# Kernel optimization log

Measured on AMD Instinct MI355X. Metric: run time of the kernel, lower is better.

## Reference

```python
import jax, jax.numpy as jnp
from jax import lax
import numpy as np

# Dims
B_, CIN, COUT, T = 2, 64, 128, 8192
K, NM, N, DCONV, EXP = 5, 2, 16, 4, 2   # kernel, n_mamba, d_state, d_conv, expand
DI = EXP * COUT                          # d_inner = 256
DTR = (COUT + 15) // 16                  # dt_rank = 8
M = NM * 2                               # mamba instances (fwd+bwd per block)


def setup_inputs() -> dict:
    key = jax.random.key(0)
    ks = jax.random.split(key, 8)
    r = lambda k, s, sc=0.02: (jax.random.normal(k, s) * sc).astype(jnp.float32)
    return {
        "x": jax.random.normal(ks[0], (B_, CIN, T), dtype=jnp.float32),
        "conv_w": r(ks[1], (COUT, CIN, K), 0.05),
        "conv_b": jnp.zeros((COUT,), jnp.float32),
        "gn_g": jnp.ones((COUT,), jnp.float32),
        "gn_b": jnp.zeros((COUT,), jnp.float32),
        "prelu_a": jnp.full((1,), 0.25, jnp.float32),
        "ln_g": jnp.ones((NM, COUT), jnp.float32),
        "ln_b": jnp.zeros((NM, COUT), jnp.float32),
        "W_in": r(ks[2], (M, 2 * DI, COUT)),
        "conv1d_w": r(ks[3], (M, DI, 1, DCONV), 0.1),
        "conv1d_b": jnp.zeros((M, DI), jnp.float32),
        "W_xproj": r(ks[4], (M, DTR + 2 * N, DI)),
        "W_dt": r(ks[5], (M, DI, DTR), 0.1),
        "b_dt": jnp.full((M, DI), -4.0, jnp.float32),
        "A_log": jnp.broadcast_to(jnp.log(jnp.arange(1, N + 1, dtype=jnp.float32)), (M, DI, N)).copy(),
        "D_param": jnp.ones((M, DI), jnp.float32),
        "W_out": r(ks[6], (M, COUT, DI)),
    }


def _silu(x):
    return x * jax.nn.sigmoid(x)


def _layernorm(x, g, b, eps=1e-5):
    mu = x.mean(-1, keepdims=True)
    v = ((x - mu) ** 2).mean(-1, keepdims=True)
    return (x - mu) * lax.rsqrt(v + eps) * g + b


def _mamba(h, Wi, cw, cb, Wx, Wd, bd, Alog, Dp, Wo):
    # h: [B, L, d_model] -> [B, L, d_model]. Standard Mamba (S6) block.
    Bb, L, _ = h.shape
    xz = jnp.einsum('bld,ed->ble', h, Wi)               # [B,L,2*DI]
    xp, z = jnp.split(xz, 2, axis=-1)
    xc = jnp.transpose(xp, (0, 2, 1))                   # [B,DI,L]
    xc = lax.conv_general_dilated(xc, cw, (1,), [(DCONV - 1, 0)],
                                  feature_group_count=DI,
                                  dimension_numbers=('NCH', 'OIH', 'NCH')) + cb[None, :, None]
    u = _silu(jnp.transpose(xc, (0, 2, 1)))             # [B,L,DI]
    xdbl = jnp.einsum('bld,ed->ble', u, Wx)             # [B,L,DTR+2N]
    dt, Bm, Cm = jnp.split(xdbl, [DTR, DTR + N], axis=-1)
    delta = jax.nn.softplus(jnp.einsum('blr,dr->bld', dt, Wd) + bd)  # [B,L,DI]
    A = -jnp.exp(Alog)                                  # [DI,N]
    dA = jnp.exp(delta[..., None] * A)                  # [B,L,DI,N]
    dBu = (delta * u)[..., None] * Bm[:, :, None, :]    # [B,L,DI,N]

    def step(hc, inp):
        a, b, c = inp
        hc = a * hc + b                                  # [B,DI,N]
        return hc, jnp.einsum('bdn,bn->bd', hc, c)

    h0 = jnp.zeros((Bb, DI, N), dtype=h.dtype)
    _, ys = lax.scan(step, h0, (jnp.moveaxis(dA, 1, 0), jnp.moveaxis(dBu, 1, 0), jnp.moveaxis(Cm, 1, 0)))
    y = jnp.moveaxis(ys, 0, 1) + u * Dp                 # [B,L,DI]
    y = y * _silu(z)
    return jnp.einsum('ble,de->bld', y, Wo)


def reference(x, conv_w, conv_b, gn_g, gn_b, prelu_a, ln_g, ln_b, W_in,
              conv1d_w, conv1d_b, W_xproj, W_dt, b_dt, A_log, D_param, W_out):
    # Conv1d stride 2, padding K//2: [B,CIN,T] -> [B,COUT,T//2]
    h = lax.conv_general_dilated(x, conv_w, (2,), [(K // 2, K // 2)],
                                 dimension_numbers=('NCH', 'OIH', 'NCH')) + conv_b[None, :, None]
    # GroupNorm(1, COUT): normalize jointly over (C, T)
    mu = h.mean((1, 2), keepdims=True)
    v = ((h - mu) ** 2).mean((1, 2), keepdims=True)
    h = (h - mu) * lax.rsqrt(v + 1e-5) * gn_g[None, :, None] + gn_b[None, :, None]
    h = jnp.where(h >= 0, h, prelu_a[0] * h)            # PReLU (shared scalar)
    h = jnp.transpose(h, (0, 2, 1))                     # [B, L, C]
    for i in range(NM):
        hn = _layernorm(h, ln_g[i], ln_b[i])
        f, bw = 2 * i, 2 * i + 1
        yf = _mamba(hn, W_in[f], conv1d_w[f], conv1d_b[f], W_xproj[f], W_dt[f], b_dt[f], A_log[f], D_param[f], W_out[f])
        hb = jnp.flip(hn, axis=1)
        yb = jnp.flip(_mamba(hb, W_in[bw], conv1d_w[bw], conv1d_b[bw], W_xproj[bw], W_dt[bw], b_dt[bw], A_log[bw], D_param[bw], W_out[bw]), axis=1)
        h = h + yf + yb                                  # bidirectional residual
    return jnp.transpose(h, (0, 2, 1))                   # [B, COUT, T//2]
```

## Files before the change

kernel.cpp:

```cpp
#include <hip/hip_runtime.h>
#include <hip/hip_bf16.h>
#include <math.h>

constexpr int B2   = 2;
constexpr int CIN  = 64;
constexpr int COUT = 128;
constexpr int T    = 8192;
constexpr int L    = 4096;
constexpr int DI   = 256;
constexpr int NST  = 16;
constexpr int DTR  = 8;
constexpr int Q    = 32;
constexpr int NC   = 128;
constexpr int TOK  = B2 * L;

typedef __attribute__((ext_vector_type(8))) short bf16x8s;
typedef __attribute__((ext_vector_type(4))) float f32x4;

__device__ __forceinline__ float sigmoidf_(float x) { return 1.f / (1.f + __expf(-x)); }
__device__ __forceinline__ unsigned short f2bf(float f) {
    unsigned int u = __float_as_uint(f);
    unsigned int r = (u + 0x7FFFu + ((u >> 16) & 1u)) >> 16;
    return (unsigned short)r;
}
__device__ __forceinline__ float bf2f(unsigned short s) {
    return __uint_as_float((unsigned int)s << 16);
}

__global__ __launch_bounds__(256) void prep_all_kernel(
    const float* __restrict__ W_in, const float* __restrict__ W_out,
    const float* __restrict__ cw,
    unsigned short* __restrict__ Winb, unsigned short* __restrict__ Woutb,
    unsigned short* __restrict__ Wrb, float* __restrict__ stats) {
    int idx = blockIdx.x * 256 + threadIdx.x;
    if (blockIdx.x == 0 && threadIdx.x < 4) stats[threadIdx.x] = 0.f;
    if (idx < 262144) {
        Winb[idx] = f2bf(W_in[idx]);
    } else if (idx < 393216) {
        int i = idx - 262144; Woutb[i] = f2bf(W_out[i]);
    } else if (idx < 434176) {
        int i = idx - 393216;
        int co = i / 320, r = i % 320;
        int kp = r >> 6, ci = r & 63;
        Wrb[i] = f2bf(cw[co * 320 + ci * 5 + kp]);
    }
}

__global__ __launch_bounds__(256) void xpose_kernel(
    const float* __restrict__ x, unsigned short* __restrict__ xTb) {
    __shared__ float tile[64][65];
    int b = blockIdx.y, tb = blockIdx.x * 64, tid = threadIdx.x;
    #pragma unroll
    for (int i = 0; i < 16; ++i) {
        int idx = i * 256 + tid; int ci = idx >> 6, tt = idx & 63;
        tile[ci][tt] = x[((size_t)b * CIN + ci) * T + tb + tt];
    }
    __syncthreads();
    #pragma unroll
    for (int i = 0; i < 16; ++i) {
        int idx = i * 256 + tid; int tt = idx >> 6, ci = idx & 63;
        xTb[((size_t)b * T + tb + tt) * 64 + ci] = f2bf(tile[ci][tt]);
    }
}

__global__ __launch_bounds__(256) void conv_mfma_kernel(
    const unsigned short* __restrict__ xTb, const unsigned short* __restrict__ Wrb,
    const float* __restrict__ cb, float* __restrict__ h, float* __restrict__ stats) {
    const int tid = threadIdx.x;
    const int w = tid >> 6, lane = tid & 63, q = lane >> 4, c = lane & 15;
    const int t0g = blockIdx.x * 64;
    const int t0  = t0g + w * 16;
    const int ct0 = blockIdx.y * 64;
    const int b   = t0g >> 12;
    const int l   = (t0 + c) & (L - 1);
    f32x4 acc[4] = {};
    for (int kc = 0; kc < 320; kc += 32) {
        int kp  = kc >> 6;
        int ci0 = (kc & 63) + q * 8;
        int p = 2 * l + kp - 2;
        bf16x8s a = {};
        if (p >= 0 && p < T)
            a = *(const bf16x8s*)&xTb[((size_t)b * T + p) * 64 + ci0];
        #pragma unroll
        for (int i = 0; i < 4; ++i) {
            bf16x8s bb = *(const bf16x8s*)&Wrb[(size_t)(ct0 + i * 16 + c) * 320 + kc + q * 8];
            acc[i] = __builtin_amdgcn_mfma_f32_16x16x32_bf16(a, bb, acc[i], 0, 0, 0);
        }
    }
    float s = 0.f, ss = 0.f;
    #pragma unroll
    for (int i = 0; i < 4; ++i) {
        int cout = ct0 + i * 16 + c;
        float bias = cb[cout];
        #pragma unroll
        for (int r = 0; r < 4; ++r) {
            int tok = t0 + q * 4 + r;
            float v = acc[i][r] + bias;
            h[(size_t)tok * COUT + cout] = v;
            s += v; ss += v * v;
        }
    }
    #pragma unroll
    for (int off = 32; off; off >>= 1) {
        s  += __shfl_down(s,  off, 64);
        ss += __shfl_down(ss, off, 64);
    }
    if (lane == 0) {
        atomicAdd(&stats[b * 2 + 0], s);
        atomicAdd(&stats[b * 2 + 1], ss);
    }
}

__global__ __launch_bounds__(256) void gn_ln_kernel(
    float* __restrict__ h, const float* __restrict__ gn_g,
    const float* __restrict__ gn_b, const float* __restrict__ prelu_a,
    const float* __restrict__ stats, unsigned short* __restrict__ hnb,
    const float* __restrict__ lng, const float* __restrict__ lnb) {
    int wave = threadIdx.x >> 6, lane = threadIdx.x & 63;
    int t = blockIdx.x * 4 + wave;
    int b = t >> 12;
    const float n = (float)(L * COUT);
    float mu   = stats[b * 2 + 0] / n;
    float var  = stats[b * 2 + 1] / n - mu * mu;
    float rstd = rsqrtf(var + 1e-5f);
    float a = prelu_a[0];
    float* row = h + (size_t)t * COUT;
    float2 v  = *(const float2*)&row[lane * 2];
    float2 g  = *(const float2*)&gn_g[lane * 2];
    float2 bb = *(const float2*)&gn_b[lane * 2];
    v.x = (v.x - mu) * rstd * g.x + bb.x; v.x = v.x >= 0.f ? v.x : a * v.x;
    v.y = (v.y - mu) * rstd * g.y + bb.y; v.y = v.y >= 0.f ? v.y : a * v.y;
    *(float2*)&row[lane * 2] = v;
    float s = v.x + v.y, ss = v.x * v.x + v.y * v.y;
    #pragma unroll
    for (int off = 32; off; off >>= 1) {
        s  += __shfl_xor(s,  off, 64);
        ss += __shfl_xor(ss, off, 64);
    }
    float mu2 = s * (1.f / 128.f);
    float var2 = ss * (1.f / 128.f) - mu2 * mu2;
    float rstd2 = rsqrtf(var2 + 1e-5f);
    float2 gg = *(const float2*)&lng[lane * 2];
    float2 lb = *(const float2*)&lnb[lane * 2];
    ushort2 o;
    o.x = f2bf((v.x - mu2) * rstd2 * gg.x + lb.x);
    o.y = f2bf((v.y - mu2) * rstd2 * gg.y + lb.y);
    *(ushort2*)&hnb[(size_t)t * COUT + lane * 2] = o;
}

__global__ __launch_bounds__(256) void ln_kernel(
    const float* __restrict__ h, unsigned short* __restrict__ hnb,
    const float* __restrict__ g, const float* __restrict__ bta) {
    int wave = threadIdx.x >> 6, lane = threadIdx.x & 63;
    int t = blockIdx.x * 4 + wave;
    const float* row = h + (size_t)t * COUT;
    float2 v = *(const float2*)&row[lane * 2];
    float s = v.x + v.y, ss = v.x * v.x + v.y * v.y;
    #pragma unroll
    for (int off = 32; off; off >>= 1) {
        s  += __shfl_xor(s,  off, 64);
        ss += __shfl_xor(ss, off, 64);
    }
    float mu = s * (1.f / 128.f);
    float var = ss * (1.f / 128.f) - mu * mu;
    float rstd = rsqrtf(var + 1e-5f);
    float2 gg = *(const float2*)&g[lane * 2];
    float2 bb = *(const float2*)&bta[lane * 2];
    ushort2 o;
    o.x = f2bf((v.x - mu) * rstd * gg.x + bb.x);
    o.y = f2bf((v.y - mu) * rstd * gg.y + bb.y);
    *(ushort2*)&hnb[(size_t)t * COUT + lane * 2] = o;
}

__global__ __launch_bounds__(256) void inproj_dw_kernel(
    const unsigned short* __restrict__ hnb, const unsigned short* __restrict__ Winb,
    const float* __restrict__ cw, const float* __restrict__ cbias,
    float* __restrict__ u0, float* __restrict__ u1,
    unsigned short* __restrict__ zb0, unsigned short* __restrict__ zb1, int layer) {
    __shared__ float xs[80 * 68];
    const int tid = threadIdx.x;
    const int w = tid >> 6, lane = tid & 63, q = lane >> 4, c = lane & 15;
    const int tBase = blockIdx.x * 64;
    const int nBase = blockIdx.y * 64;
    const int inst = nBase >> 9;
    const int e0 = nBase & 511;
    const int m = layer * 2 + inst;
    const unsigned short* Wb = Winb + (size_t)m * 512 * 128;

    if (e0 >= 256) {
        const int t0 = tBase + w * 16;
        f32x4 acc[4] = {};
        for (int kc = 0; kc < 128; kc += 32) {
            bf16x8s a = *(const bf16x8s*)&hnb[(size_t)(t0 + c) * 128 + kc + q * 8];
            #pragma unroll
            for (int i = 0; i < 4; ++i) {
                bf16x8s bb = *(const bf16x8s*)&Wb[(size_t)(e0 + i * 16 + c) * 128 + kc + q * 8];
                acc[i] = __builtin_amdgcn_mfma_f32_16x16x32_bf16(a, bb, acc[i], 0, 0, 0);
            }
        }
        unsigned short* zb = inst ? zb1 : zb0;
        #pragma unroll
        for (int i = 0; i < 4; ++i) {
            int eo = (e0 + i * 16 + c) & 255;
            #pragma unroll
            for (int r = 0; r < 4; ++r) {
                int tok = t0 + q * 4 + r;
                float v = acc[i][r];
                zb[(size_t)tok * DI + eo] = f2bf(v * sigmoidf_(v));
            }
        }
        return;
    }
    const int winT0 = (inst == 0) ? (tBase - 16) : tBase;
    for (int pass = 0; pass < 2; ++pass) {
        if (pass == 1 && w != 0) break;
        int slot = (pass == 0) ? (w + (inst == 0 ? 1 : 0))
                               : ((inst == 0) ? 0 : 4);
        int tokA = winT0 + slot * 16 + c;
        tokA = tokA < 0 ? 0 : (tokA > TOK - 1 ? TOK - 1 : tokA);
        f32x4 acc[4] = {};
        for (int kc = 0; kc < 128; kc += 32) {
            bf16x8s a = *(const bf16x8s*)&hnb[(size_t)tokA * 128 + kc + q * 8];
            #pragma unroll
            for (int i = 0; i < 4; ++i) {
                bf16x8s bb = *(const bf16x8s*)&Wb[(size_t)(e0 + i * 16 + c) * 128 + kc + q * 8];
                acc[i] = __builtin_amdgcn_mfma_f32_16x16x32_bf16(a, bb, acc[i], 0, 0, 0);
            }
        }
        #pragma unroll
        for (int i = 0; i < 4; ++i)
            #pragma unroll
            for (int r = 0; r < 4; ++r)
                xs[(slot * 16 + q * 4 + r) * 68 + i * 16 + c] = acc[i][r];
    }
    __syncthreads();
    const int l0base = tBase & (L - 1);
    const int ch4 = tid & 15;
    const int d0 = e0 + ch4 * 4;
    float4 w0 = *(const float4*)&cw[(size_t)(m * DI + d0 + 0) * 4];
    float4 w1 = *(const float4*)&cw[(size_t)(m * DI + d0 + 1) * 4];
    float4 w2 = *(const float4*)&cw[(size_t)(m * DI + d0 + 2) * 4];
    float4 w3 = *(const float4*)&cw[(size_t)(m * DI + d0 + 3) * 4];
    float4 bias4 = *(const float4*)&cbias[m * DI + d0];
    float* ud = inst ? u1 : u0;
    #pragma unroll
    for (int p = 0; p < 4; ++p) {
        int j = p * 16 + (tid >> 4);
        float4 acc = bias4;
        #pragma unroll
        for (int k = 0; k < 4; ++k) {
            bool valid = (inst == 0) ? (l0base + j - 3 + k >= 0)
                                     : (l0base + j + 3 - k < L);
            if (valid) {
                int wj = (inst == 0) ? (j + 13 + k) : (j + 3 - k);
                float4 v = *(const float4*)&xs[wj * 68 + ch4 * 4];
                float wk0 = ((const float*)&w0)[k], wk1 = ((const float*)&w1)[k];
                float wk2 = ((const float*)&w2)[k], wk3 = ((const float*)&w3)[k];
                acc.x = fmaf(wk0, v.x, acc.x); acc.y = fmaf(wk1, v.y, acc.y);
                acc.z = fmaf(wk2, v.z, acc.z); acc.w = fmaf(wk3, v.w, acc.w);
            }
        }
        acc.x *= sigmoidf_(acc.x); acc.y *= sigmoidf_(acc.y);
        acc.z *= sigmoidf_(acc.z); acc.w *= sigmoidf_(acc.w);
        *(float4*)&ud[(size_t)(tBase + j) * DI + d0] = acc;
    }
}

__global__ __launch_bounds__(256) void xproj_kernel(
    const float* __restrict__ u0, const float* __restrict__ u1,
    const float* __restrict__ Wx, const float* __restrict__ Wdt,
    const float* __restrict__ bdt,
    float* __restrict__ dl0, float* __restrict__ dl1,
    float* __restrict__ Bm0, float* __restrict__ Bm1,
    float* __restrict__ Cm0, float* __restrict__ Cm1, int layer) {
    __shared__ float Ws[40 * 132];
    __shared__ float As[128 * 33];
    __shared__ float xd[32 * 9];
    const int tid   = threadIdx.x;
    const int tBase = blockIdx.x * 32;
    const int inst  = blockIdx.y;
    const int m     = layer * 2 + inst;
    const float* u  = inst ? u1 : u0;
    const float* Wm = Wx + (size_t)m * 40 * 256;
    const int t  = tid & 31;
    const int eq = tid >> 5;
    float acc[5] = {};
    for (int kc = 0; kc < 256; kc += 128) {
        __syncthreads();
        #pragma unroll
        for (int i = 0; i < 5; ++i) {
            int idx = i * 256 + tid;
            int e = idx >> 5, kq = idx & 31;
            float4 w4 = *(const float4*)&Wm[(size_t)e * 256 + kc + kq * 4];
            float* dstw = &Ws[e * 132 + kq * 4];
            dstw[0] = w4.x; dstw[1] = w4.y; dstw[2] = w4.z; dstw[3] = w4.w;
        }
        #pragma unroll
        for (int i = 0; i < 4; ++i) {
            int flat = i * 256 + tid;
            int tt = flat >> 5, kq = flat & 31;
            float4 v = *(const float4*)&u[(size_t)(tBase + tt) * DI + kc + kq * 4];
            As[(kq * 4 + 0) * 33 + tt] = v.x;
            As[(kq * 4 + 1) * 33 + tt] = v.y;
            As[(kq * 4 + 2) * 33 + tt] = v.z;
            As[(kq * 4 + 3) * 33 + tt] = v.w;
        }
        __syncthreads();
        #pragma unroll 4
        for (int kk = 0; kk < 128; ++kk) {
            float a = As[kk * 33 + t];
            acc[0] = fmaf(a, Ws[(eq     ) * 132 + kk], acc[0]);
            acc[1] = fmaf(a, Ws[(eq +  8) * 132 + kk], acc[1]);
            acc[2] = fmaf(a, Ws[(eq + 16) * 132 + kk], acc[2]);
            acc[3] = fmaf(a, Ws[(eq + 24) * 132 + kk], acc[3]);
            acc[4] = fmaf(a, Ws[(eq + 32) * 132 + kk], acc[4]);
        }
    }
    {
        int tok = tBase + t;
        float* Bm = inst ? Bm1 : Bm0;
        float* Cm = inst ? Cm1 : Cm0;
        xd[t * 9 + eq] = acc[0];
        Bm[(size_t)tok * NST + eq]     = acc[1];
        Bm[(size_t)tok * NST + 8 + eq] = acc[2];
        Cm[(size_t)tok * NST + eq]     = acc[3];
        Cm[(size_t)tok * NST + 8 + eq] = acc[4];
    }
    __syncthreads();
    {
        int d = tid;
        float wr[8];
        #pragma unroll
        for (int r = 0; r < 8; ++r) wr[r] = Wdt[((size_t)m * DI + d) * DTR + r];
        float bb = bdt[m * DI + d];
        float* dl = inst ? dl1 : dl0;
        #pragma unroll 4
        for (int tt = 0; tt < 32; ++tt) {
            float a2 = bb;
            #pragma unroll
            for (int r = 0; r < 8; ++r) a2 = fmaf(xd[tt * 9 + r], wr[r], a2);
            float sp = fmaxf(a2, 0.f) + __logf(1.f + __expf(-fabsf(a2)));
            dl[(size_t)(tBase + tt) * DI + d] = sp;
        }
    }
}

__global__ __launch_bounds__(256) void scan1_kernel(
    const float* __restrict__ dl0, const float* __restrict__ dl1,
    const float* __restrict__ u0,  const float* __restrict__ u1,
    const float* __restrict__ Bm0, const float* __restrict__ Bm1,
    const float* __restrict__ A_log,
    float* __restrict__ hend, float* __restrict__ dsumb, int layer) {
    const int tid = threadIdx.x;
    const int nq = tid & 3, dlane = tid >> 2;
    const int chunk = blockIdx.x & (NC - 1), dtile = blockIdx.x >> 7;
    const int b = blockIdx.y, inst = blockIdx.z;
    const int m = layer * 2 + inst, dir = inst;
    const int d = dtile * 64 + dlane;
    const float* dl = inst ? dl1 : dl0;
    const float* u  = inst ? u1  : u0;
    const float* Bm = inst ? Bm1 : Bm0;
    float4 av = *(const float4*)&A_log[((size_t)m * DI + d) * NST + nq * 4];
    const float a0 = -expf(av.x), a1 = -expf(av.y), a2 = -expf(av.z), a3 = -expf(av.w);
    const int s0 = chunk * Q;
    const int l0 = dir ? (L - 1 - s0) : s0;
    const int stp = dir ? -1 : 1;
    long iDU = ((long)(b * L + l0)) * DI + d;
    int  iB  = ((b * L + l0) << 4) + nq * 4;
    const long sDU = (long)stp * DI;
    const int  sB  = stp * NST;
    float h0 = 0.f, h1 = 0.f, h2 = 0.f, h3 = 0.f, dsum = 0.f;
    #pragma unroll 4
    for (int t = 0; t < Q; ++t) {
        float dlt = dl[iDU], uu = u[iDU];
        float4 bm = *(const float4*)&Bm[iB];
        float du = dlt * uu;
        h0 = fmaf(__expf(dlt * a0), h0, du * bm.x);
        h1 = fmaf(__expf(dlt * a1), h1, du * bm.y);
        h2 = fmaf(__expf(dlt * a2), h2, du * bm.z);
        h3 = fmaf(__expf(dlt * a3), h3, du * bm.w);
        dsum += dlt;
        iDU += sDU; iB += sB;
    }
    size_t oh = (((size_t)(inst * 2 + b) * DI + d) * NC + chunk) * NST + nq * 4;
    *(float4*)&hend[oh] = make_float4(h0, h1, h2, h3);
    if (nq == 0) dsumb[((size_t)(inst * 2 + b) * NC + chunk) * DI + d] = dsum;
}

__global__ __launch_bounds__(256) void combine_kernel(
    float* __restrict__ hend, const float* __restrict__ dsumb,
    const float* __restrict__ A_log, int layer) {
    int flat = blockIdx.x * 256 + threadIdx.x;
    int n = flat & 15;
    int d = (flat >> 4) & 255;
    int b = (flat >> 12) & 1;
    int inst = flat >> 13;
    int m = layer * 2 + inst;
    float a = -expf(A_log[((size_t)m * DI + d) * NST + n]);
    size_t baseE = (((size_t)(inst * 2 + b) * DI + d) * NC) * NST + n;
    size_t baseD = ((size_t)(inst * 2 + b) * NC) * DI + d;
    float hc = 0.f;
    #pragma unroll 4
    for (int c = 0; c < NC; ++c) {
        float tmp = hend[baseE + (size_t)c * NST];
        hend[baseE + (size_t)c * NST] = hc;
        float ds = dsumb[baseD + (size_t)c * DI];
        hc = fmaf(__expf(a * ds), hc, tmp);
    }
}

__global__ __launch_bounds__(256) void scan2_kernel(
    const float* __restrict__ dl0, const float* __restrict__ dl1,
    const float* __restrict__ u0,  const float* __restrict__ u1,
    const float* __restrict__ Bm0, const float* __restrict__ Bm1,
    const float* __restrict__ Cm0, const float* __restrict__ Cm1,
    unsigned short* __restrict__ zb0, unsigned short* __restrict__ zb1,
    const float* __restrict__ hin, const float* __restrict__ A_log,
    const float* __restrict__ Dp, int layer) {
    const int tid = threadIdx.x;
    const int nq = tid & 3, dlane = tid >> 2;
    const int chunk = blockIdx.x & (NC - 1), dtile = blockIdx.x >> 7;
    const int b = blockIdx.y, inst = blockIdx.z;
    const int m = layer * 2 + inst, dir = inst;
    const int d = dtile * 64 + dlane;
    const float* dl = inst ? dl1 : dl0;
    const float* u  = inst ? u1  : u0;
    const float* Bm = inst ? Bm1 : Bm0;
    const float* Cm = inst ? Cm1 : Cm0;
    unsigned short* zs = inst ? zb1 : zb0;
    float4 av = *(const float4*)&A_log[((size_t)m * DI + d) * NST + nq * 4];
    const float a0 = -expf(av.x), a1 = -expf(av.y), a2 = -expf(av.z), a3 = -expf(av.w);
    const float dpar = Dp[m * DI + d];
    const int s0 = chunk * Q;
    const int l0 = dir ? (L - 1 - s0) : s0;
    const int stp = dir ? -1 : 1;
    long iDU = ((long)(b * L + l0)) * DI + d;
    int  iB  = ((b * L + l0) << 4) + nq * 4;
    const long sDU = (long)stp * DI;
    const int  sB  = stp * NST;
    float4 hv = *(const float4*)&hin[(((size_t)(inst * 2 + b) * DI + d) * NC + chunk) * NST + nq * 4];
    float h0 = hv.x, h1 = hv.y, h2 = hv.z, h3 = hv.w;
    #pragma unroll 4
    for (int t = 0; t < Q; ++t) {
        float dlt = dl[iDU], uu = u[iDU];
        float4 bm = *(const float4*)&Bm[iB];
        float4 cm = *(const float4*)&Cm[iB];
        float du = dlt * uu;
        h0 = fmaf(__expf(dlt * a0), h0, du * bm.x);
        h1 = fmaf(__expf(dlt * a1), h1, du * bm.y);
        h2 = fmaf(__expf(dlt * a2), h2, du * bm.z);
        h3 = fmaf(__expf(dlt * a3), h3, du * bm.w);
        float yp = h0 * cm.x + h1 * cm.y + h2 * cm.z + h3 * cm.w;
        yp += __shfl_xor(yp, 1, 4);
        yp += __shfl_xor(yp, 2, 4);
        if (nq == 0) {
            float zv = bf2f(zs[iDU]);
            zs[iDU] = f2bf(fmaf(uu, dpar, yp) * zv);
        }
        iDU += sDU; iB += sB;
    }
}

__global__ __launch_bounds__(256) void outproj_mfma_kernel(
    const unsigned short* __restrict__ ygb0, const unsigned short* __restrict__ ygb1,
    const unsigned short* __restrict__ Woutb, float* __restrict__ h,
    float* __restrict__ out, int layer) {
    const int tid = threadIdx.x;
    const int w = tid >> 6, lane = tid & 63, q = lane >> 4, c = lane & 15;
    const int t0 = blockIdx.x * 64 + w * 16;
    const int ct0 = blockIdx.y * 32;
    f32x4 acc[2] = {};
    #pragma unroll
    for (int inst = 0; inst < 2; ++inst) {
        const unsigned short* yg = inst ? ygb1 : ygb0;
        const unsigned short* Wb = Woutb + (size_t)(layer * 2 + inst) * COUT * DI;
        for (int kc = 0; kc < 256; kc += 32) {
            bf16x8s a = *(const bf16x8s*)&yg[(size_t)(t0 + c) * DI + kc + q * 8];
            #pragma unroll
            for (int i = 0; i < 2; ++i) {
                bf16x8s bb = *(const bf16x8s*)&Wb[(size_t)(ct0 + i * 16 + c) * DI + kc + q * 8];
                acc[i] = __builtin_amdgcn_mfma_f32_16x16x32_bf16(a, bb, acc[i], 0, 0, 0);
            }
        }
    }
    if (layer == 0) {
        #pragma unroll
        for (int i = 0; i < 2; ++i) {
            int cout = ct0 + i * 16 + c;
            #pragma unroll
            for (int r = 0; r < 4; ++r) {
                int tok = t0 + q * 4 + r;
                h[(size_t)tok * COUT + cout] += acc[i][r];
            }
        }
    } else {
        int tok0 = t0 + q * 4;
        int b = tok0 >> 12, l = tok0 & (L - 1);
        #pragma unroll
        for (int i = 0; i < 2; ++i) {
            int cout = ct0 + i * 16 + c;
            float4 o;
            o.x = h[(size_t)(tok0 + 0) * COUT + cout] + acc[i][0];
            o.y = h[(size_t)(tok0 + 1) * COUT + cout] + acc[i][1];
            o.z = h[(size_t)(tok0 + 2) * COUT + cout] + acc[i][2];
            o.w = h[(size_t)(tok0 + 3) * COUT + cout] + acc[i][3];
            *(float4*)&out[((size_t)(b * COUT + cout)) * L + l] = o;
        }
    }
}

extern "C" void kernel_launch(void* const* d_in, const int* in_sizes, int n_in,
                              void* d_out, int out_size, void* d_ws, size_t ws_size,
                              hipStream_t stream) {
    const float* x        = (const float*)d_in[0];
    const float* conv_w   = (const float*)d_in[1];
    const float* conv_b   = (const float*)d_in[2];
    const float* gn_g     = (const float*)d_in[3];
    const float* gn_b     = (const float*)d_in[4];
    const float* prelu_a  = (const float*)d_in[5];
    const float* ln_g     = (const float*)d_in[6];
    const float* ln_b     = (const float*)d_in[7];
    const float* W_in     = (const float*)d_in[8];
    const float* conv1d_w = (const float*)d_in[9];
    const float* conv1d_b = (const float*)d_in[10];
    const float* W_xproj  = (const float*)d_in[11];
    const float* W_dt     = (const float*)d_in[12];
    const float* b_dt     = (const float*)d_in[13];
    const float* A_log    = (const float*)d_in[14];
    const float* D_param  = (const float*)d_in[15];
    const float* W_out    = (const float*)d_in[16];

    float* ws = (float*)d_ws;
    float* h     = ws;
    unsigned short* zb0 = (unsigned short*)(ws + 5242880);
    unsigned short* zb1 = (unsigned short*)(ws + 6291456);
    float* u0    = ws + 7340032;
    float* u1    = ws + 9437184;
    float* dl0   = ws + 11534336;
    float* dl1   = ws + 13631488;
    float* Bm0   = ws + 15728640;
    float* Bm1   = ws + 15859712;
    float* Cm0   = ws + 15990784;
    float* Cm1   = ws + 16121856;
    float* hend  = ws + 16252928;
    float* dsumb = ws + 18350080;
    unsigned short* Winb  = (unsigned short*)(ws + 18481152);
    unsigned short* Wrb   = (unsigned short*)(ws + 18612224);
    unsigned short* Woutb = (unsigned short*)(ws + 18632704);
    float* stats = ws + 18698240;
    unsigned short* hnb = (unsigned short*)hend;
    unsigned short* xTb = zb0;
    float* out = (float*)d_out;

    prep_all_kernel<<<1696, 256, 0, stream>>>(W_in, W_out, conv_w, Winb, Woutb, Wrb, stats);
    xpose_kernel<<<dim3(T / 64, B2), 256, 0, stream>>>(x, xTb);
    conv_mfma_kernel<<<dim3(TOK / 64, COUT / 64), 256, 0, stream>>>(xTb, Wrb, conv_b, h, stats);
    gn_ln_kernel<<<TOK / 4, 256, 0, stream>>>(h, gn_g, gn_b, prelu_a, stats, hnb, ln_g, ln_b);

    for (int layer = 0; layer < 2; ++layer) {
        if (layer == 1)
            ln_kernel<<<TOK / 4, 256, 0, stream>>>(h, hnb, ln_g + COUT, ln_b + COUT);
        inproj_dw_kernel<<<dim3(TOK / 64, 16), 256, 0, stream>>>(hnb, Winb, conv1d_w, conv1d_b,
                                                                 u0, u1, zb0, zb1, layer);
        xproj_kernel<<<dim3(TOK / 32, 2), 256, 0, stream>>>(u0, u1, W_xproj, W_dt, b_dt,
                                                            dl0, dl1, Bm0, Bm1, Cm0, Cm1, layer);
        scan1_kernel<<<dim3(NC * 4, B2, 2), 256, 0, stream>>>(dl0, dl1, u0, u1, Bm0, Bm1,
                                                              A_log, hend, dsumb, layer);
        combine_kernel<<<64, 256, 0, stream>>>(hend, dsumb, A_log, layer);
        scan2_kernel<<<dim3(NC * 4, B2, 2), 256, 0, stream>>>(dl0, dl1, u0, u1, Bm0, Bm1, Cm0, Cm1,
                                                              zb0, zb1, hend, A_log, D_param, layer);
        outproj_mfma_kernel<<<dim3(TOK / 64, 4), 256, 0, stream>>>(zb0, zb1, Woutb, h, out, layer);
    }
}
```

Measured before the change: 377.6 us.

## Fuse chunk-local scan pass into xproj kernel

Result: no change. 374.1 us (-0.9%).

```diff
diff --git a/kernel.cpp b/kernel.cpp
--- a/kernel.cpp
+++ b/kernel.cpp
@@ -269,13 +269,15 @@
 __global__ __launch_bounds__(256) void xproj_kernel(
     const float* __restrict__ u0, const float* __restrict__ u1,
     const float* __restrict__ Wx, const float* __restrict__ Wdt,
-    const float* __restrict__ bdt,
+    const float* __restrict__ bdt, const float* __restrict__ A_log,
     float* __restrict__ dl0, float* __restrict__ dl1,
     float* __restrict__ Bm0, float* __restrict__ Bm1,
-    float* __restrict__ Cm0, float* __restrict__ Cm1, int layer) {
+    float* __restrict__ Cm0, float* __restrict__ Cm1,
+    float* __restrict__ hend, float* __restrict__ dsumb, int layer) {
     __shared__ float Ws[40 * 132];
     __shared__ float As[128 * 33];
     __shared__ float xd[32 * 9];
+    __shared__ float bmL[32][17];
     const int tid   = threadIdx.x;
     const int tBase = blockIdx.x * 32;
     const int inst  = blockIdx.y;
@@ -321,6 +323,8 @@
         float* Bm = inst ? Bm1 : Bm0;
         float* Cm = inst ? Cm1 : Cm0;
         xd[t * 9 + eq] = acc[0];
+        bmL[t][eq]     = acc[1];
+        bmL[t][8 + eq] = acc[2];
         Bm[(size_t)tok * NST + eq]     = acc[1];
         Bm[(size_t)tok * NST + 8 + eq] = acc[2];
         Cm[(size_t)tok * NST + eq]     = acc[3];
@@ -328,63 +332,42 @@
     }
     __syncthreads();
     {
-        int d = tid;
+        const int d = tid;
         float wr[8];
         #pragma unroll
         for (int r = 0; r < 8; ++r) wr[r] = Wdt[((size_t)m * DI + d) * DTR + r];
         float bb = bdt[m * DI + d];
         float* dl = inst ? dl1 : dl0;
-        #pragma unroll 4
-        for (int tt = 0; tt < 32; ++tt) {
+        float a[16];
+        #pragma unroll
+        for (int n = 0; n < 16; ++n)
+            a[n] = -expf(A_log[((size_t)m * DI + d) * NST + n]);
+        float hst[16] = {};
+        float dsum = 0.f;
+        const int b    = tBase >> 12;
+        const int tile = (tBase & (L - 1)) >> 5;
+        const int chunk = inst ? (NC - 1 - tile) : tile;
+        for (int s = 0; s < Q; ++s) {
+            int tt = inst ? (Q - 1 - s) : s;
             float a2 = bb;
             #pragma unroll
             for (int r = 0; r < 8; ++r) a2 = fmaf(xd[tt * 9 + r], wr[r], a2);
             float sp = fmaxf(a2, 0.f) + __logf(1.f + __expf(-fabsf(a2)));
-            dl[(size_t)(tBase + tt) * DI + d] = sp;
-        }
-    }
-}
-
-__global__ __launch_bounds__(256) void scan1_kernel(
-    const float* __restrict__ dl0, const float* __restrict__ dl1,
-    const float* __restrict__ u0,  const float* __restrict__ u1,
-    const float* __restrict__ Bm0, const float* __restrict__ Bm1,
-    const float* __restrict__ A_log,
-    float* __restrict__ hend, float* __restrict__ dsumb, int layer) {
-    const int tid = threadIdx.x;
-    const int nq = tid & 3, dlane = tid >> 2;
-    const int chunk = blockIdx.x & (NC - 1), dtile = blockIdx.x >> 7;
-    const int b = blockIdx.y, inst = blockIdx.z;
-    const int m = layer * 2 + inst, dir = inst;
-    const int d = dtile * 64 + dlane;
-    const float* dl = inst ? dl1 : dl0;
-    const float* u  = inst ? u1  : u0;
-    const float* Bm = inst ? Bm1 : Bm0;
-    float4 av = *(const float4*)&A_log[((size_t)m * DI + d) * NST + nq * 4];
-    const float a0 = -expf(av.x), a1 = -expf(av.y), a2 = -expf(av.z), a3 = -expf(av.w);
-    const int s0 = chunk * Q;
-    const int l0 = dir ? (L - 1 - s0) : s0;
-    const int stp = dir ? -1 : 1;
-    long iDU = ((long)(b * L + l0)) * DI + d;
-    int  iB  = ((b * L + l0) << 4) + nq * 4;
-    const long sDU = (long)stp * DI;
-    const int  sB  = stp * NST;
-    float h0 = 0.f, h1 = 0.f, h2 = 0.f, h3 = 0.f, dsum = 0.f;
-    #pragma unroll 4
-    for (int t = 0; t < Q; ++t) {
-        float dlt = dl[iDU], uu = u[iDU];
-        float4 bm = *(const float4*)&Bm[iB];
-        float du = dlt * uu;
-        h0 = fmaf(__expf(dlt * a0), h0, du * bm.x);
-        h1 = fmaf(__expf(dlt * a1), h1, du * bm.y);
-        h2 = fmaf(__expf(dlt * a2), h2, du * bm.z);
-        h3 = fmaf(__expf(dlt * a3), h3, du * bm.w);
-        dsum += dlt;
-        iDU += sDU; iB += sB;
-    }
-    size_t oh = (((size_t)(inst * 2 + b) * DI + d) * NC + chunk) * NST + nq * 4;
-    *(float4*)&hend[oh] = make_float4(h0, h1, h2, h3);
-    if (nq == 0) dsumb[((size_t)(inst * 2 + b) * NC + chunk) * DI + d] = dsum;
+            size_t gi = (size_t)(tBase + tt) * DI + d;
+            dl[gi] = sp;
+            float uu = u[gi];
+            float du = sp * uu;
+            dsum += sp;
+            #pragma unroll
+            for (int n = 0; n < 16; ++n)
+                hst[n] = fmaf(__expf(sp * a[n]), hst[n], du * bmL[tt][n]);
+        }
+        size_t oh = (((size_t)(inst * 2 + b) * DI + d) * NC + chunk) * NST;
+        #pragma unroll
+        for (int n = 0; n < 16; n += 4)
+            *(float4*)&hend[oh + n] = make_float4(hst[n], hst[n+1], hst[n+2], hst[n+3]);
+        dsumb[((size_t)(inst * 2 + b) * NC + chunk) * DI + d] = dsum;
+    }
 }
 
 __global__ __launch_bounds__(256) void combine_kernel(
@@ -562,10 +545,9 @@
             ln_kernel<<<TOK / 4, 256, 0, stream>>>(h, hnb, ln_g + COUT, ln_b + COUT);
         inproj_dw_kernel<<<dim3(TOK / 64, 16), 256, 0, stream>>>(hnb, Winb, conv1d_w, conv1d_b,
                                                                  u0, u1, zb0, zb1, layer);
-        xproj_kernel<<<dim3(TOK / 32, 2), 256, 0, stream>>>(u0, u1, W_xproj, W_dt, b_dt,
-                                                            dl0, dl1, Bm0, Bm1, Cm0, Cm1, layer);
-        scan1_kernel<<<dim3(NC * 4, B2, 2), 256, 0, stream>>>(dl0, dl1, u0, u1, Bm0, Bm1,
-                                                              A_log, hend, dsumb, layer);
+        xproj_kernel<<<dim3(TOK / 32, 2), 256, 0, stream>>>(u0, u1, W_xproj, W_dt, b_dt, A_log,
+                                                            dl0, dl1, Bm0, Bm1, Cm0, Cm1,
+                                                            hend, dsumb, layer);
         combine_kernel<<<64, 256, 0, stream>>>(hend, dsumb, A_log, layer);
         scan2_kernel<<<dim3(NC * 4, B2, 2), 256, 0, stream>>>(dl0, dl1, u0, u1, Bm0, Bm1, Cm0, Cm1,
                                                               zb0, zb1, hend, A_log, D_param, layer);
```
